# Performance work log

Hardware: AMD Instinct MI355X
Metric: run time of the kernel (lower is better)

The kernel has to match this reference:

```python
import jax, jax.numpy as jnp
import numpy as np

MARGIN = 0.3
PD_EPS = 1e-6  # torch.nn.functional.pairwise_distance default eps (added to the diff)


def setup_inputs() -> dict:
    key = jax.random.key(0)
    k1, k2 = jax.random.split(key)
    n, d = 8192, 128
    inputs = jax.random.normal(k1, (n, d), dtype=jnp.float32)
    positive = jax.random.normal(k2, (n, d), dtype=jnp.float32)
    return {"inputs": inputs, "positive": positive}


def reference(inputs, positive):
    # Pairwise squared Euclidean distances: ||xi||^2 + ||xj||^2 - 2 xi.xj  -> [n, n]
    sq = jnp.sum(inputs * inputs, axis=1, keepdims=True)  # [n, 1]
    dist = sq + sq.T - 2.0 * (inputs @ inputs.T)
    dist = jnp.sqrt(jnp.clip(dist, 1e-12, None))

    # Original: dist[i].argsort()[4] -> 5th-nearest (index 0 is self at ~0 distance).
    # Equivalent, avoiding full per-row sort: top-5 smallest distances.
    _, idx = jax.lax.top_k(-dist, 5)  # idx: [n, 5], ascending by distance
    negative = inputs[idx[:, 4]]  # hard negatives, [n, d]

    # TripletMarginLoss(margin=0.3, p=2): pairwise_distance adds eps to the diff.
    d_ap = jnp.linalg.norm(inputs - positive + PD_EPS, axis=1)
    d_an = jnp.linalg.norm(inputs - negative + PD_EPS, axis=1)
    return jnp.mean(jnp.maximum(d_ap - d_an + MARGIN, 0.0))
```

## Files before the change

### kernel.cpp

```cpp
#include <hip/hip_runtime.h>

#define NN 8192
#define DD 128
#define CH 16
#define CPC (NN / CH)
#define TILES (CPC / 64)
#define NPART 64

typedef __bf16 bf16x8 __attribute__((ext_vector_type(8)));
typedef float f32x4 __attribute__((ext_vector_type(4)));

#define PACK_INIT __uint_as_float(0xFF7FFFFFu)

static __device__ __forceinline__ float packsi(float s, unsigned idx) {
  return __uint_as_float((__float_as_uint(s) & 0xFFFFE000u) | idx);
}

#define NET4(S0, S1, S2, S3, v)                                                \
  {                                                                            \
    float v_ = (v), o0 = S0, o1 = S1, o2 = S2;                                 \
    S0 = fmaxf(o0, v_);                                                        \
    S1 = __builtin_amdgcn_fmed3f(v_, o0, o1);                                  \
    S2 = __builtin_amdgcn_fmed3f(v_, o1, o2);                                  \
    S3 = __builtin_amdgcn_fmed3f(v_, o2, S3);                                  \
  }
#define NET5(S0, S1, S2, S3, S4, v)                                            \
  {                                                                            \
    float v_ = (v), o0 = S0, o1 = S1, o2 = S2, o3 = S3;                        \
    S0 = fmaxf(o0, v_);                                                        \
    S1 = __builtin_amdgcn_fmed3f(v_, o0, o1);                                  \
    S2 = __builtin_amdgcn_fmed3f(v_, o1, o2);                                  \
    S3 = __builtin_amdgcn_fmed3f(v_, o2, o3);                                  \
    S4 = __builtin_amdgcn_fmed3f(v_, o3, S4);                                  \
  }

static __device__ __forceinline__ unsigned short f2bf(float f) {
  unsigned u = __float_as_uint(f);
  u += 0x7FFFu + ((u >> 16) & 1u);
  return (unsigned short)(u >> 16);
}

static __device__ __forceinline__ void gload_lds16(const void* g, void* l) {
  __builtin_amdgcn_global_load_lds(
      (const __attribute__((address_space(1))) unsigned*)g,
      (__attribute__((address_space(3))) unsigned*)l, 16, 0, 0);
}

__global__ __launch_bounds__(256) void prep_kernel(const float* __restrict__ x,
                                                   unsigned short* __restrict__ xb,
                                                   float* __restrict__ sq,
                                                   float* __restrict__ partial) {
  const int wave = threadIdx.x >> 6, lane = threadIdx.x & 63;
  const int row = blockIdx.x * 4 + wave;
  const float2 v = ((const float2*)(x + (size_t)row * DD))[lane];
  float ss = v.x * v.x + v.y * v.y;
#pragma unroll
  for (int off = 32; off; off >>= 1) ss += __shfl_down(ss, off);
  if (lane == 0) sq[row] = fmaf(-0.5f, ss, -70.0f);
  unsigned packed = (unsigned)f2bf(v.x) | ((unsigned)f2bf(v.y) << 16);
  ((unsigned*)(xb + (size_t)row * DD))[lane] = packed;
  if (blockIdx.x == 0 && threadIdx.x < NPART) partial[threadIdx.x] = 0.0f;
}

__global__ __launch_bounds__(256, 2) void dist_topk_kernel(
    const unsigned short* __restrict__ xb, const float* __restrict__ sq,
    float* __restrict__ pscore) {
  const int t = threadIdx.x;
  const int wave = t >> 6, lane = t & 63;
  const int lrow = lane & 15, lquad = lane >> 4;
  const int rowBase = blockIdx.x * 256;
  const int chunk = blockIdx.y;
  const int j0 = chunk * CPC;
  const bool hasDiag = ((blockIdx.x >> 1) == (int)blockIdx.y);

  __shared__ unsigned short colsB[2][64 * DD];
  __shared__ float sqs_all[CPC];

  const int r0 = rowBase + wave * 64 + lrow;
  const unsigned short* ap0 = xb + (size_t)(r0)*DD + lquad * 8;
  const unsigned short* ap1 = xb + (size_t)(r0 + 16) * DD + lquad * 8;
  const unsigned short* ap2 = xb + (size_t)(r0 + 32) * DD + lquad * 8;
  const unsigned short* ap3 = xb + (size_t)(r0 + 48) * DD + lquad * 8;
  bf16x8 a00 = *(const bf16x8*)(ap0), a01 = *(const bf16x8*)(ap0 + 32),
         a02 = *(const bf16x8*)(ap0 + 64), a03 = *(const bf16x8*)(ap0 + 96);
  bf16x8 a10 = *(const bf16x8*)(ap1), a11 = *(const bf16x8*)(ap1 + 32),
         a12 = *(const bf16x8*)(ap1 + 64), a13 = *(const bf16x8*)(ap1 + 96);
  bf16x8 a20 = *(const bf16x8*)(ap2), a21 = *(const bf16x8*)(ap2 + 32),
         a22 = *(const bf16x8*)(ap2 + 64), a23 = *(const bf16x8*)(ap2 + 96);
  bf16x8 a30 = *(const bf16x8*)(ap3), a31 = *(const bf16x8*)(ap3 + 32),
         a32 = *(const bf16x8*)(ap3 + 64), a33 = *(const bf16x8*)(ap3 + 96);

  float q00 = PACK_INIT, q01 = PACK_INIT, q02 = PACK_INIT, q03 = PACK_INIT,
        q04 = PACK_INIT;
  float q10 = PACK_INIT, q11 = PACK_INIT, q12 = PACK_INIT, q13 = PACK_INIT,
        q14 = PACK_INIT;
  float q20 = PACK_INIT, q21 = PACK_INIT, q22 = PACK_INIT, q23 = PACK_INIT,
        q24 = PACK_INIT;
  float q30 = PACK_INIT, q31 = PACK_INIT, q32 = PACK_INIT, q33 = PACK_INIT,
        q34 = PACK_INIT;

  const int psl = (t & ~15) | ((t ^ (t >> 4)) & 15);

#define ISSUE_TILE(buf, jtrow)                                                 \
  {                                                                            \
    const float4* s_ = (const float4*)(xb + (size_t)(jtrow)*DD);               \
    char* l_ = (char*)(&colsB[buf][0]) + wave * 1024;                          \
    gload_lds16(s_ + psl, l_);                                                 \
    gload_lds16(s_ + psl + 256, l_ + 4096);                                    \
    gload_lds16(s_ + psl + 512, l_ + 8192);                                    \
    gload_lds16(s_ + psl + 768, l_ + 12288);                                   \
  }

  sqs_all[t] = sq[j0 + t];
  sqs_all[t + 256] = sq[j0 + 256 + t];
  ISSUE_TILE(0, j0)

#define KBODY(INSROW)                                                          \
  for (int it = 0; it < TILES; ++it) {                                         \
    const int jt = j0 + it * 64;                                               \
    const int cur = it & 1;                                                    \
    __syncthreads();          \
    if (it + 1 < TILES) { ISSUE_TILE(cur ^ 1, jt + 64) }                       \
    _Pragma("unroll")                                                          \
    for (int ct = 0; ct < 4; ++ct) {                                           \
      const unsigned short* bb = &colsB[cur][(ct * 16 + lrow) * DD];           \
      bf16x8 b0 = *(const bf16x8*)(bb + (((0 + lquad) ^ lrow) << 3));          \
      bf16x8 b1 = *(const bf16x8*)(bb + (((4 + lquad) ^ lrow) << 3));          \
      bf16x8 b2 = *(const bf16x8*)(bb + (((8 + lquad) ^ lrow) << 3));          \
      bf16x8 b3 = *(const bf16x8*)(bb + (((12 + lquad) ^ lrow) << 3));         \
      const f32x4 nsq4 = *(const f32x4*)&sqs_all[it * 64 + ct * 16 + lquad * 4];\
      f32x4 ac0 = __builtin_amdgcn_mfma_f32_16x16x32_bf16(b0, a00, nsq4, 0, 0, 0);\
      f32x4 ac1 = __builtin_amdgcn_mfma_f32_16x16x32_bf16(b0, a10, nsq4, 0, 0, 0);\
      f32x4 ac2 = __builtin_amdgcn_mfma_f32_16x16x32_bf16(b0, a20, nsq4, 0, 0, 0);\
      f32x4 ac3 = __builtin_amdgcn_mfma_f32_16x16x32_bf16(b0, a30, nsq4, 0, 0, 0);\
      ac0 = __builtin_amdgcn_mfma_f32_16x16x32_bf16(b1, a01, ac0, 0, 0, 0);    \
      ac1 = __builtin_amdgcn_mfma_f32_16x16x32_bf16(b1, a11, ac1, 0, 0, 0);    \
      ac2 = __builtin_amdgcn_mfma_f32_16x16x32_bf16(b1, a21, ac2, 0, 0, 0);    \
      ac3 = __builtin_amdgcn_mfma_f32_16x16x32_bf16(b1, a31, ac3, 0, 0, 0);    \
      ac0 = __builtin_amdgcn_mfma_f32_16x16x32_bf16(b2, a02, ac0, 0, 0, 0);    \
      ac1 = __builtin_amdgcn_mfma_f32_16x16x32_bf16(b2, a12, ac1, 0, 0, 0);    \
      ac2 = __builtin_amdgcn_mfma_f32_16x16x32_bf16(b2, a22, ac2, 0, 0, 0);    \
      ac3 = __builtin_amdgcn_mfma_f32_16x16x32_bf16(b2, a32, ac3, 0, 0, 0);    \
      ac0 = __builtin_amdgcn_mfma_f32_16x16x32_bf16(b3, a03, ac0, 0, 0, 0);    \
      ac1 = __builtin_amdgcn_mfma_f32_16x16x32_bf16(b3, a13, ac1, 0, 0, 0);    \
      ac2 = __builtin_amdgcn_mfma_f32_16x16x32_bf16(b3, a23, ac2, 0, 0, 0);    \
      ac3 = __builtin_amdgcn_mfma_f32_16x16x32_bf16(b3, a33, ac3, 0, 0, 0);    \
      const unsigned colb = (unsigned)(jt + ct * 16 + lquad * 4);              \
      _Pragma("unroll")                                                        \
      for (int r = 0; r < 4; ++r) {                                            \
        const unsigned cr = colb + r;                                          \
        INSROW(0, packsi(ac0[r], cr));                                         \
        INSROW(1, packsi(ac1[r], cr));                                         \
        INSROW(2, packsi(ac2[r], cr));                                         \
        INSROW(3, packsi(ac3[r], cr));                                         \
      }                                                                        \
    }                                                                          \
  }

#define INS4(G, V) NET4(q##G##0, q##G##1, q##G##2, q##G##3, (V))
#define INS5(G, V) NET5(q##G##0, q##G##1, q##G##2, q##G##3, q##G##4, (V))

  if (hasDiag) {
    KBODY(INS5)
  } else {
    KBODY(INS4)
  }
#undef KBODY

#define MERGE4(G, M)                                                           \
  {                                                                            \
    float o0 = __shfl_xor(q##G##0, M), o1 = __shfl_xor(q##G##1, M),            \
          o2 = __shfl_xor(q##G##2, M), o3 = __shfl_xor(q##G##3, M);            \
    NET4(q##G##0, q##G##1, q##G##2, q##G##3, o0);                              \
    NET4(q##G##0, q##G##1, q##G##2, q##G##3, o1);                              \
    NET4(q##G##0, q##G##1, q##G##2, q##G##3, o2);                              \
    NET4(q##G##0, q##G##1, q##G##2, q##G##3, o3);                              \
  }
#define MERGE5(G, M)                                                           \
  {                                                                            \
    float o0 = __shfl_xor(q##G##0, M), o1 = __shfl_xor(q##G##1, M),            \
          o2 = __shfl_xor(q##G##2, M), o3 = __shfl_xor(q##G##3, M),            \
          o4 = __shfl_xor(q##G##4, M);                                         \
    NET5(q##G##0, q##G##1, q##G##2, q##G##3, q##G##4, o0);                     \
    NET5(q##G##0, q##G##1, q##G##2, q##G##3, q##G##4, o1);                     \
    NET5(q##G##0, q##G##1, q##G##2, q##G##3, q##G##4, o2);                     \
    NET5(q##G##0, q##G##1, q##G##2, q##G##3, q##G##4, o3);                     \
    NET5(q##G##0, q##G##1, q##G##2, q##G##3, q##G##4, o4);                     \
  }
  if (hasDiag) {
    MERGE5(0, 16) MERGE5(1, 16) MERGE5(2, 16) MERGE5(3, 16)
    MERGE5(0, 32) MERGE5(1, 32) MERGE5(2, 32) MERGE5(3, 32)
  } else {
    MERGE4(0, 16) MERGE4(1, 16) MERGE4(2, 16) MERGE4(3, 16)
    MERGE4(0, 32) MERGE4(1, 32) MERGE4(2, 32) MERGE4(3, 32)
  }

  if (lquad == 0) {
    float* b0p = pscore + (size_t)(r0)*80 + chunk * 5;
    b0p[0] = q00; b0p[1] = q01; b0p[2] = q02; b0p[3] = q03; b0p[4] = q04;
    float* b1p = pscore + (size_t)(r0 + 16) * 80 + chunk * 5;
    b1p[0] = q10; b1p[1] = q11; b1p[2] = q12; b1p[3] = q13; b1p[4] = q14;
    float* b2p = pscore + (size_t)(r0 + 32) * 80 + chunk * 5;
    b2p[0] = q20; b2p[1] = q21; b2p[2] = q22; b2p[3] = q23; b2p[4] = q24;
    float* b3p = pscore + (size_t)(r0 + 48) * 80 + chunk * 5;
    b3p[0] = q30; b3p[1] = q31; b3p[2] = q32; b3p[3] = q33; b3p[4] = q34;
  }
}

__global__ __launch_bounds__(256) void final_kernel(const float* __restrict__ x,
                                                    const float* __restrict__ pos,
                                                    const float* __restrict__ pscore,
                                                    float* __restrict__ partial) {
  const int wave = threadIdx.x >> 6, lane = threadIdx.x & 63;
  const int row = blockIdx.x * 4 + wave;

  const float2 xv  = ((const float2*)(x   + (size_t)row  * DD))[lane];
  const float2 pv  = ((const float2*)(pos + (size_t)row  * DD))[lane];

  float q0 = PACK_INIT, q1 = PACK_INIT, q2 = PACK_INIT, q3 = PACK_INIT,
        q4 = PACK_INIT;
  if (lane < CH) {
    const float* b = pscore + (size_t)row * 80 + lane * 5;
    q0 = b[0]; q1 = b[1]; q2 = b[2]; q3 = b[3]; q4 = b[4];
  }
#pragma unroll
  for (int m = 1; m < CH; m <<= 1) {
    float o0 = __shfl_xor(q0, m), o1 = __shfl_xor(q1, m), o2 = __shfl_xor(q2, m),
          o3 = __shfl_xor(q3, m), o4 = __shfl_xor(q4, m);
    NET5(q0, q1, q2, q3, q4, o0);
    NET5(q0, q1, q2, q3, q4, o1);
    NET5(q0, q1, q2, q3, q4, o2);
    NET5(q0, q1, q2, q3, q4, o3);
    NET5(q0, q1, q2, q3, q4, o4);
  }
  const int nidx = (int)(__float_as_uint(__shfl(q4, 0)) & 0x1FFFu);

  const float2 nvv = ((const float2*)(x + (size_t)nidx * DD))[lane];
  float a0 = xv.x - pv.x + 1e-6f, a1 = xv.y - pv.y + 1e-6f;
  float b0 = xv.x - nvv.x + 1e-6f, b1 = xv.y - nvv.y + 1e-6f;
  float dap = a0 * a0 + a1 * a1;
  float dan = b0 * b0 + b1 * b1;
#pragma unroll
  for (int off = 32; off; off >>= 1) {
    dap += __shfl_down(dap, off);
    dan += __shfl_down(dan, off);
  }
  __shared__ float hs[4];
  if (lane == 0) hs[wave] = fmaxf(sqrtf(dap) - sqrtf(dan) + 0.3f, 0.0f);
  __syncthreads();
  if (threadIdx.x == 0) {
    float s = hs[0] + hs[1] + hs[2] + hs[3];
    atomicAdd(&partial[blockIdx.x & (NPART - 1)], s);
  }
}

__global__ __launch_bounds__(64) void reduce_kernel(const float* __restrict__ partial,
                                                    float* __restrict__ out) {
  float v = partial[threadIdx.x];
#pragma unroll
  for (int off = 32; off; off >>= 1) v += __shfl_down(v, off);
  if (threadIdx.x == 0) out[0] = v * (1.0f / 8192.0f);
}

extern "C" void kernel_launch(void* const* d_in, const int* in_sizes, int n_in,
                              void* d_out, int out_size, void* d_ws, size_t ws_size,
                              hipStream_t stream) {
  const float* x   = (const float*)d_in[0];
  const float* pos = (const float*)d_in[1];
  float* out = (float*)d_out;

  char* w = (char*)d_ws;
  unsigned short* xb = (unsigned short*)w;
  float* sq = (float*)(w + (size_t)NN * DD * 2);
  float* pscore = (float*)(w + (size_t)NN * DD * 2 + (size_t)NN * 4);
  float* partial = (float*)(w + (size_t)NN * DD * 2 + (size_t)NN * 4 +
                            (size_t)NN * 80 * 4);

  prep_kernel<<<NN / 4, 256, 0, stream>>>(x, xb, sq, partial);
  dist_topk_kernel<<<dim3(NN / 256, CH), 256, 0, stream>>>(xb, sq, pscore);
  final_kernel<<<NN / 4, 256, 0, stream>>>(x, pos, pscore, partial);
  reduce_kernel<<<1, 64, 0, stream>>>(partial, out);
}
```

Before: 104.2 us.

## Fuse all four kernels into one cooperative persistent kernel with grid syncs

Adds a cooperative mega_kernel that runs prep, distance/top-k, final loss and reduction in one launch, separated by grid-wide syncs, with 512 blocks each doing several rows of the prep and final phases. The aim is to remove three kernel launch gaps and the tail idle time between dependent stages. It keeps the old multi-kernel path as a fallback when occupancy or the cooperative launch fails. The grid syncs and the requirement that all 512 blocks be co-resident add their own cost, and the prep and final phases lose parallelism per block.

```diff
diff --git a/kernel.cpp b/kernel.cpp
--- a/kernel.cpp
+++ b/kernel.cpp
@@ -1,4 +1,7 @@
 #include <hip/hip_runtime.h>
+#include <hip/hip_cooperative_groups.h>
+
+namespace cg = cooperative_groups;
 
 #define NN 8192
 #define DD 128
@@ -46,61 +49,6 @@
       (__attribute__((address_space(3))) unsigned*)l, 16, 0, 0);
 }
 
-__global__ __launch_bounds__(256) void prep_kernel(const float* __restrict__ x,
-                                                   unsigned short* __restrict__ xb,
-                                                   float* __restrict__ sq,
-                                                   float* __restrict__ partial) {
-  const int wave = threadIdx.x >> 6, lane = threadIdx.x & 63;
-  const int row = blockIdx.x * 4 + wave;
-  const float2 v = ((const float2*)(x + (size_t)row * DD))[lane];
-  float ss = v.x * v.x + v.y * v.y;
-#pragma unroll
-  for (int off = 32; off; off >>= 1) ss += __shfl_down(ss, off);
-  if (lane == 0) sq[row] = fmaf(-0.5f, ss, -70.0f);
-  unsigned packed = (unsigned)f2bf(v.x) | ((unsigned)f2bf(v.y) << 16);
-  ((unsigned*)(xb + (size_t)row * DD))[lane] = packed;
-  if (blockIdx.x == 0 && threadIdx.x < NPART) partial[threadIdx.x] = 0.0f;
-}
-
-__global__ __launch_bounds__(256, 2) void dist_topk_kernel(
-    const unsigned short* __restrict__ xb, const float* __restrict__ sq,
-    float* __restrict__ pscore) {
-  const int t = threadIdx.x;
-  const int wave = t >> 6, lane = t & 63;
-  const int lrow = lane & 15, lquad = lane >> 4;
-  const int rowBase = blockIdx.x * 256;
-  const int chunk = blockIdx.y;
-  const int j0 = chunk * CPC;
-  const bool hasDiag = ((blockIdx.x >> 1) == (int)blockIdx.y);
-
-  __shared__ unsigned short colsB[2][64 * DD];
-  __shared__ float sqs_all[CPC];
-
-  const int r0 = rowBase + wave * 64 + lrow;
-  const unsigned short* ap0 = xb + (size_t)(r0)*DD + lquad * 8;
-  const unsigned short* ap1 = xb + (size_t)(r0 + 16) * DD + lquad * 8;
-  const unsigned short* ap2 = xb + (size_t)(r0 + 32) * DD + lquad * 8;
-  const unsigned short* ap3 = xb + (size_t)(r0 + 48) * DD + lquad * 8;
-  bf16x8 a00 = *(const bf16x8*)(ap0), a01 = *(const bf16x8*)(ap0 + 32),
-         a02 = *(const bf16x8*)(ap0 + 64), a03 = *(const bf16x8*)(ap0 + 96);
-  bf16x8 a10 = *(const bf16x8*)(ap1), a11 = *(const bf16x8*)(ap1 + 32),
-         a12 = *(const bf16x8*)(ap1 + 64), a13 = *(const bf16x8*)(ap1 + 96);
-  bf16x8 a20 = *(const bf16x8*)(ap2), a21 = *(const bf16x8*)(ap2 + 32),
-         a22 = *(const bf16x8*)(ap2 + 64), a23 = *(const bf16x8*)(ap2 + 96);
-  bf16x8 a30 = *(const bf16x8*)(ap3), a31 = *(const bf16x8*)(ap3 + 32),
-         a32 = *(const bf16x8*)(ap3 + 64), a33 = *(const bf16x8*)(ap3 + 96);
-
-  float q00 = PACK_INIT, q01 = PACK_INIT, q02 = PACK_INIT, q03 = PACK_INIT,
-        q04 = PACK_INIT;
-  float q10 = PACK_INIT, q11 = PACK_INIT, q12 = PACK_INIT, q13 = PACK_INIT,
-        q14 = PACK_INIT;
-  float q20 = PACK_INIT, q21 = PACK_INIT, q22 = PACK_INIT, q23 = PACK_INIT,
-        q24 = PACK_INIT;
-  float q30 = PACK_INIT, q31 = PACK_INIT, q32 = PACK_INIT, q33 = PACK_INIT,
-        q34 = PACK_INIT;
-
-  const int psl = (t & ~15) | ((t ^ (t >> 4)) & 15);
-
 #define ISSUE_TILE(buf, jtrow)                                                 \
   {                                                                            \
     const float4* s_ = (const float4*)(xb + (size_t)(jtrow)*DD);               \
@@ -110,10 +58,6 @@
     gload_lds16(s_ + psl + 512, l_ + 8192);                                    \
     gload_lds16(s_ + psl + 768, l_ + 12288);                                   \
   }
-
-  sqs_all[t] = sq[j0 + t];
-  sqs_all[t + 256] = sq[j0 + 256 + t];
-  ISSUE_TILE(0, j0)
 
 #define KBODY(INSROW)                                                          \
   for (int it = 0; it < TILES; ++it) {                                         \
@@ -160,13 +104,6 @@
 #define INS4(G, V) NET4(q##G##0, q##G##1, q##G##2, q##G##3, (V))
 #define INS5(G, V) NET5(q##G##0, q##G##1, q##G##2, q##G##3, q##G##4, (V))
 
-  if (hasDiag) {
-    KBODY(INS5)
-  } else {
-    KBODY(INS4)
-  }
-#undef KBODY
-
 #define MERGE4(G, M)                                                           \
   {                                                                            \
     float o0 = __shfl_xor(q##G##0, M), o1 = __shfl_xor(q##G##1, M),            \
@@ -187,24 +124,88 @@
     NET5(q##G##0, q##G##1, q##G##2, q##G##3, q##G##4, o3);                     \
     NET5(q##G##0, q##G##1, q##G##2, q##G##3, q##G##4, o4);                     \
   }
-  if (hasDiag) {
-    MERGE5(0, 16) MERGE5(1, 16) MERGE5(2, 16) MERGE5(3, 16)
-    MERGE5(0, 32) MERGE5(1, 32) MERGE5(2, 32) MERGE5(3, 32)
-  } else {
-    MERGE4(0, 16) MERGE4(1, 16) MERGE4(2, 16) MERGE4(3, 16)
-    MERGE4(0, 32) MERGE4(1, 32) MERGE4(2, 32) MERGE4(3, 32)
-  }
-
-  if (lquad == 0) {
-    float* b0p = pscore + (size_t)(r0)*80 + chunk * 5;
-    b0p[0] = q00; b0p[1] = q01; b0p[2] = q02; b0p[3] = q03; b0p[4] = q04;
-    float* b1p = pscore + (size_t)(r0 + 16) * 80 + chunk * 5;
-    b1p[0] = q10; b1p[1] = q11; b1p[2] = q12; b1p[3] = q13; b1p[4] = q14;
-    float* b2p = pscore + (size_t)(r0 + 32) * 80 + chunk * 5;
-    b2p[0] = q20; b2p[1] = q21; b2p[2] = q22; b2p[3] = q23; b2p[4] = q24;
-    float* b3p = pscore + (size_t)(r0 + 48) * 80 + chunk * 5;
-    b3p[0] = q30; b3p[1] = q31; b3p[2] = q32; b3p[3] = q33; b3p[4] = q34;
-  }
+
+#define PHASE_D_BODY                                                           \
+  {                                                                            \
+    const int lrow = lane & 15, lquad = lane >> 4;                             \
+    const int rowBase = blockIdx.x * 256;                                      \
+    const int chunk = blockIdx.y;                                              \
+    const int j0 = chunk * CPC;                                                \
+    const bool hasDiag = ((blockIdx.x >> 1) == (int)blockIdx.y);               \
+    const int r0 = rowBase + wave * 64 + lrow;                                 \
+    const unsigned short* ap0 = xb + (size_t)(r0)*DD + lquad * 8;              \
+    const unsigned short* ap1 = xb + (size_t)(r0 + 16) * DD + lquad * 8;       \
+    const unsigned short* ap2 = xb + (size_t)(r0 + 32) * DD + lquad * 8;       \
+    const unsigned short* ap3 = xb + (size_t)(r0 + 48) * DD + lquad * 8;       \
+    bf16x8 a00 = *(const bf16x8*)(ap0), a01 = *(const bf16x8*)(ap0 + 32),      \
+           a02 = *(const bf16x8*)(ap0 + 64), a03 = *(const bf16x8*)(ap0 + 96); \
+    bf16x8 a10 = *(const bf16x8*)(ap1), a11 = *(const bf16x8*)(ap1 + 32),      \
+           a12 = *(const bf16x8*)(ap1 + 64), a13 = *(const bf16x8*)(ap1 + 96); \
+    bf16x8 a20 = *(const bf16x8*)(ap2), a21 = *(const bf16x8*)(ap2 + 32),      \
+           a22 = *(const bf16x8*)(ap2 + 64), a23 = *(const bf16x8*)(ap2 + 96); \
+    bf16x8 a30 = *(const bf16x8*)(ap3), a31 = *(const bf16x8*)(ap3 + 32),      \
+           a32 = *(const bf16x8*)(ap3 + 64), a33 = *(const bf16x8*)(ap3 + 96); \
+    float q00 = PACK_INIT, q01 = PACK_INIT, q02 = PACK_INIT, q03 = PACK_INIT,  \
+          q04 = PACK_INIT;                                                     \
+    float q10 = PACK_INIT, q11 = PACK_INIT, q12 = PACK_INIT, q13 = PACK_INIT,  \
+          q14 = PACK_INIT;                                                     \
+    float q20 = PACK_INIT, q21 = PACK_INIT, q22 = PACK_INIT, q23 = PACK_INIT,  \
+          q24 = PACK_INIT;                                                     \
+    float q30 = PACK_INIT, q31 = PACK_INIT, q32 = PACK_INIT, q33 = PACK_INIT,  \
+          q34 = PACK_INIT;                                                     \
+    const int psl = (t & ~15) | ((t ^ (t >> 4)) & 15);                         \
+    sqs_all[t] = sq[j0 + t];                                                   \
+    sqs_all[t + 256] = sq[j0 + 256 + t];                                       \
+    ISSUE_TILE(0, j0)                                                          \
+    if (hasDiag) {                                                             \
+      KBODY(INS5)                                                              \
+    } else {                                                                   \
+      KBODY(INS4)                                                              \
+    }                                                                          \
+    if (hasDiag) {                                                             \
+      MERGE5(0, 16) MERGE5(1, 16) MERGE5(2, 16) MERGE5(3, 16)                  \
+      MERGE5(0, 32) MERGE5(1, 32) MERGE5(2, 32) MERGE5(3, 32)                  \
+    } else {                                                                   \
+      MERGE4(0, 16) MERGE4(1, 16) MERGE4(2, 16) MERGE4(3, 16)                  \
+      MERGE4(0, 32) MERGE4(1, 32) MERGE4(2, 32) MERGE4(3, 32)                  \
+    }                                                                          \
+    if (lquad == 0) {                                                          \
+      float* b0p = pscore + (size_t)(r0)*80 + chunk * 5;                       \
+      b0p[0] = q00; b0p[1] = q01; b0p[2] = q02; b0p[3] = q03; b0p[4] = q04;    \
+      float* b1p = pscore + (size_t)(r0 + 16) * 80 + chunk * 5;                \
+      b1p[0] = q10; b1p[1] = q11; b1p[2] = q12; b1p[3] = q13; b1p[4] = q14;    \
+      float* b2p = pscore + (size_t)(r0 + 32) * 80 + chunk * 5;                \
+      b2p[0] = q20; b2p[1] = q21; b2p[2] = q22; b2p[3] = q23; b2p[4] = q24;    \
+      float* b3p = pscore + (size_t)(r0 + 48) * 80 + chunk * 5;                \
+      b3p[0] = q30; b3p[1] = q31; b3p[2] = q32; b3p[3] = q33; b3p[4] = q34;    \
+    }                                                                          \
+  }
+
+
+__global__ __launch_bounds__(256) void prep_kernel(const float* __restrict__ x,
+                                                   unsigned short* __restrict__ xb,
+                                                   float* __restrict__ sq,
+                                                   float* __restrict__ partial) {
+  const int wave = threadIdx.x >> 6, lane = threadIdx.x & 63;
+  const int row = blockIdx.x * 4 + wave;
+  const float2 v = ((const float2*)(x + (size_t)row * DD))[lane];
+  float ss = v.x * v.x + v.y * v.y;
+#pragma unroll
+  for (int off = 32; off; off >>= 1) ss += __shfl_down(ss, off);
+  if (lane == 0) sq[row] = fmaf(-0.5f, ss, -70.0f);
+  unsigned packed = (unsigned)f2bf(v.x) | ((unsigned)f2bf(v.y) << 16);
+  ((unsigned*)(xb + (size_t)row * DD))[lane] = packed;
+  if (blockIdx.x == 0 && threadIdx.x < NPART) partial[threadIdx.x] = 0.0f;
+}
+
+__global__ __launch_bounds__(256, 2) void dist_topk_kernel(
+    const unsigned short* __restrict__ xb, const float* __restrict__ sq,
+    float* __restrict__ pscore) {
+  const int t = threadIdx.x;
+  const int wave = t >> 6, lane = t & 63;
+  __shared__ unsigned short colsB[2][64 * DD];
+  __shared__ float sqs_all[CPC];
+  PHASE_D_BODY
 }
 
 __global__ __launch_bounds__(256) void final_kernel(const float* __restrict__ x,
@@ -262,6 +263,99 @@
   if (threadIdx.x == 0) out[0] = v * (1.0f / 8192.0f);
 }
 
+
+__global__ __launch_bounds__(256, 2) void mega_kernel(
+    const float* __restrict__ x, const float* __restrict__ pos,
+    unsigned short* __restrict__ xb, float* __restrict__ sq,
+    float* __restrict__ pscore, float* __restrict__ partial,
+    float* __restrict__ out) {
+  cg::grid_group grid = cg::this_grid();
+  const int t = threadIdx.x;
+  const int wave = t >> 6, lane = t & 63;
+  const int bid = (int)blockIdx.y * 32 + (int)blockIdx.x;
+
+  __shared__ unsigned short colsB[2][64 * DD];
+  __shared__ float sqs_all[CPC];
+  __shared__ float hs[4];
+
+#pragma unroll
+  for (int i = 0; i < 4; ++i) {
+    const int row = 16 * bid + i * 4 + wave;
+    const float2 v = ((const float2*)(x + (size_t)row * DD))[lane];
+    float ss = v.x * v.x + v.y * v.y;
+#pragma unroll
+    for (int off = 32; off; off >>= 1) ss += __shfl_down(ss, off);
+    if (lane == 0) sq[row] = fmaf(-0.5f, ss, -70.0f);
+    unsigned packed = (unsigned)f2bf(v.x) | ((unsigned)f2bf(v.y) << 16);
+    ((unsigned*)(xb + (size_t)row * DD))[lane] = packed;
+  }
+  if (bid == 0 && t < NPART) partial[t] = 0.0f;
+
+  __threadfence();
+  grid.sync();
+
+  PHASE_D_BODY
+
+  __threadfence();
+  grid.sync();
+
+#pragma unroll 1
+  for (int g = 0; g < 4; ++g) {
+    const int ob = 4 * bid + g;
+    const int row = ob * 4 + wave;
+
+    const float2 xv = ((const float2*)(x + (size_t)row * DD))[lane];
+    const float2 pv = ((const float2*)(pos + (size_t)row * DD))[lane];
+
+    float q0 = PACK_INIT, q1 = PACK_INIT, q2 = PACK_INIT, q3 = PACK_INIT,
+          q4 = PACK_INIT;
+    if (lane < CH) {
+      const float* b = pscore + (size_t)row * 80 + lane * 5;
+      q0 = b[0]; q1 = b[1]; q2 = b[2]; q3 = b[3]; q4 = b[4];
+    }
+#pragma unroll
+    for (int m = 1; m < CH; m <<= 1) {
+      float o0 = __shfl_xor(q0, m), o1 = __shfl_xor(q1, m),
+            o2 = __shfl_xor(q2, m), o3 = __shfl_xor(q3, m),
+            o4 = __shfl_xor(q4, m);
+      NET5(q0, q1, q2, q3, q4, o0);
+      NET5(q0, q1, q2, q3, q4, o1);
+      NET5(q0, q1, q2, q3, q4, o2);
+      NET5(q0, q1, q2, q3, q4, o3);
+      NET5(q0, q1, q2, q3, q4, o4);
+    }
+    const int nidx = (int)(__float_as_uint(__shfl(q4, 0)) & 0x1FFFu);
+
+    const float2 nvv = ((const float2*)(x + (size_t)nidx * DD))[lane];
+    float a0 = xv.x - pv.x + 1e-6f, a1 = xv.y - pv.y + 1e-6f;
+    float b0 = xv.x - nvv.x + 1e-6f, b1 = xv.y - nvv.y + 1e-6f;
+    float dap = a0 * a0 + a1 * a1;
+    float dan = b0 * b0 + b1 * b1;
+#pragma unroll
+    for (int off = 32; off; off >>= 1) {
+      dap += __shfl_down(dap, off);
+      dan += __shfl_down(dan, off);
+    }
+    if (lane == 0) hs[wave] = fmaxf(sqrtf(dap) - sqrtf(dan) + 0.3f, 0.0f);
+    __syncthreads();
+    if (t == 0) {
+      float s = hs[0] + hs[1] + hs[2] + hs[3];
+      atomicAdd(&partial[ob & (NPART - 1)], s);
+    }
+    __syncthreads();
+  }
+
+  __threadfence();
+  grid.sync();
+
+  if (bid == 0 && t < 64) {
+    float v = atomicAdd(&partial[t], 0.0f);
+#pragma unroll
+    for (int off = 32; off; off >>= 1) v += __shfl_down(v, off);
+    if (t == 0) out[0] = v * (1.0f / 8192.0f);
+  }
+}
+
 extern "C" void kernel_launch(void* const* d_in, const int* in_sizes, int n_in,
                               void* d_out, int out_size, void* d_ws, size_t ws_size,
                               hipStream_t stream) {
@@ -276,6 +370,25 @@
   float* partial = (float*)(w + (size_t)NN * DD * 2 + (size_t)NN * 4 +
                             (size_t)NN * 80 * 4);
 
+  static int coop_state = -1;
+  if (coop_state == -1) {
+    int nb = 0;
+    hipError_t qe = hipOccupancyMaxActiveBlocksPerMultiprocessor(
+        &nb, (const void*)mega_kernel, 256, 0);
+    coop_state = (qe == hipSuccess && nb >= 2) ? 1 : 0;
+    if (coop_state == 0) (void)hipGetLastError();
+  }
+  if (coop_state == 1) {
+    void* args[] = {(void*)&x, (void*)&pos, (void*)&xb, (void*)&sq,
+                    (void*)&pscore, (void*)&partial, (void*)&out};
+    hipError_t le = hipLaunchCooperativeKernel((const void*)mega_kernel,
+                                               dim3(32, 16), dim3(256), args,
+                                               0, stream);
+    if (le == hipSuccess) return;
+    (void)hipGetLastError();
+    coop_state = 0;
+  }
+
   prep_kernel<<<NN / 4, 256, 0, stream>>>(x, xb, sq, partial);
   dist_topk_kernel<<<dim3(NN / 256, CH), 256, 0, stream>>>(xb, sq, pscore);
   final_kernel<<<NN / 4, 256, 0, stream>>>(x, pos, pscore, partial);
```

New measurement: 105.0 us. Within noise of the previous version (+0.8%).
